# Kernel tuning notes

Hardware: AMD Instinct MI355X
Metric: run time of the kernel (lower is better)

The kernel has to match this reference:

```python
import jax, jax.numpy as jnp
import numpy as np

# dims: L layers, T steps, N envs, D d_model, H heads, DH d_head, M mem_len, DI d_inner
L, T, N, D, H, DH, M, DI = 6, 128, 32, 1024, 16, 64, 128, 4096


def _layer_norm(x, g, b, eps=1e-5):
    mu = jnp.mean(x, axis=-1, keepdims=True)
    var = jnp.mean(jnp.square(x - mu), axis=-1, keepdims=True)
    return (x - mu) * jax.lax.rsqrt(var + eps) * g + b


def _rel_shift(x):
    # x: (n, h, q, k) with k axis indexed by relative distance (k-1 .. 0)
    n, h, q, k = x.shape
    x = jnp.pad(x, ((0, 0), (0, 0), (0, 0), (1, 0)))
    x = x.reshape(n, h, k + 1, q)[:, :, 1:, :].reshape(n, h, q, k)
    return x


def setup_inputs() -> dict:
    key = jax.random.key(0)
    ks = jax.random.split(key, 16)
    s = 0.02
    inp = {
        "x": jax.random.normal(ks[0], (T * N, D), jnp.float32),
        "context": jax.random.normal(ks[1], (T * N, D), jnp.float32),
        "mems": jax.random.normal(ks[2], (L, N, M, D), jnp.float32),
        "masks": jnp.ones((T * N,), jnp.float32),
        "Wq": jax.random.normal(ks[3], (L, D, H * DH), jnp.float32) * s,
        "Wk": jax.random.normal(ks[4], (L, D, H * DH), jnp.float32) * s,
        "Wv": jax.random.normal(ks[5], (L, D, H * DH), jnp.float32) * s,
        "Wr": jax.random.normal(ks[6], (L, D, H * DH), jnp.float32) * s,
        "Wo": jax.random.normal(ks[7], (L, H * DH, D), jnp.float32) * s,
        "W1": jax.random.normal(ks[8], (L, D, DI), jnp.float32) * s,
        "b1": jnp.zeros((L, DI), jnp.float32),
        "W2": jax.random.normal(ks[9], (L, DI, D), jnp.float32) * s,
        "b2": jnp.zeros((L, D), jnp.float32),
        "ln1_g": jnp.ones((L, D), jnp.float32),
        "ln1_b": jnp.zeros((L, D), jnp.float32),
        "ln2_g": jnp.ones((L, D), jnp.float32),
        "ln2_b": jnp.zeros((L, D), jnp.float32),
        "r_w_bias": jax.random.normal(ks[10], (H, DH), jnp.float32) * s,
        "r_r_bias": jax.random.normal(ks[11], (H, DH), jnp.float32) * s,
    }
    return inp


def reference(x, context, mems, masks, Wq, Wk, Wv, Wr, Wo, W1, b1, W2, b2,
              ln1_g, ln1_b, ln2_g, ln2_b, r_w_bias, r_r_bias):
    n = mems.shape[1]
    t = x.shape[0] // n
    m = mems.shape[2]
    klen = m + t
    dh = r_w_bias.shape[-1]
    h_heads = r_w_bias.shape[0]

    xs = x.reshape(t, n, -1)
    ctx = context.reshape(t, n, -1)
    mk = masks.reshape(t, n)

    # zero memories for envs that reset at the first step (mems * masks)
    mems = mems * mk[0][None, :, None, None]

    # episode-reset attention mask: token i attends token j iff j<=i and no
    # reset (mask==0) happened between them; memory visible only before any reset
    ep = jnp.cumsum((mk == 0.0).astype(jnp.int32), axis=0)  # (t, n)
    epT = ep.T  # (n, t)
    causal = jnp.tril(jnp.ones((t, t), bool))
    allow_seq = causal[None, :, :] & (epT[:, :, None] == epT[:, None, :])  # (n,t,t)
    allow_mem = jnp.broadcast_to((epT == 0)[:, :, None], (n, t, m))  # (n,t,m)
    allow = jnp.concatenate([allow_mem, allow_seq], axis=-1)[:, None]  # (n,1,t,K)

    # sinusoidal relative position embedding, distances klen-1 .. 0
    pos = jnp.arange(klen - 1, -1, -1, dtype=x.dtype)
    inv_freq = 1.0 / (10000.0 ** (jnp.arange(0, xs.shape[-1], 2, dtype=x.dtype) / xs.shape[-1]))
    ang = pos[:, None] * inv_freq[None, :]
    R = jnp.concatenate([jnp.sin(ang), jnp.cos(ang)], axis=-1)  # (K, D)

    h = xs + ctx  # fuse observation features with goal context
    scale = 1.0 / jnp.sqrt(jnp.asarray(dh, x.dtype))

    n_layer = mems.shape[0]
    for l in range(n_layer):
        cat = jnp.concatenate([jnp.transpose(mems[l], (1, 0, 2)), h], axis=0)  # (K,n,D)
        q = (h @ Wq[l]).reshape(t, n, h_heads, dh)
        k = (cat @ Wk[l]).reshape(klen, n, h_heads, dh)
        v = (cat @ Wv[l]).reshape(klen, n, h_heads, dh)
        r = (R @ Wr[l]).reshape(klen, h_heads, dh)
        AC = jnp.einsum('inhd,jnhd->nhij', q + r_w_bias, k)
        BD = _rel_shift(jnp.einsum('inhd,jhd->nhij', q + r_r_bias, r))
        score = (AC + BD) * scale
        score = jnp.where(allow, score, -1e9)
        attn = jax.nn.softmax(score, axis=-1)
        o = jnp.einsum('nhij,jnhd->inhd', attn, v).reshape(t, n, h_heads * dh) @ Wo[l]
        h = _layer_norm(h + o, ln1_g[l], ln1_b[l])
        f = jax.nn.relu(h @ W1[l] + b1[l]) @ W2[l] + b2[l]
        h = _layer_norm(h + f, ln2_g[l], ln2_b[l])

    return h.reshape(t * n, -1)
```

## Files before the change

### kernel.cpp

```cpp
#include <hip/hip_runtime.h>
#include <stdint.h>

#define DEV static __device__ __forceinline__

typedef __attribute__((ext_vector_type(4))) float f32x4;
typedef __attribute__((ext_vector_type(8))) short bf16x8;
typedef __attribute__((ext_vector_type(4))) short s16x4;

static constexpr int L_ = 6, T_ = 128, NE = 32, D_ = 1024, H_ = 16, DH_ = 64, M_ = 128, DI_ = 4096;
static constexpr int KLEN = M_ + T_;
static constexpr int TN = T_ * NE;
static constexpr int NB = NE * H_;

DEV unsigned short f2bf(float f) {
  unsigned u = __builtin_bit_cast(unsigned, f);
  u += 0x7FFFu + ((u >> 16) & 1u);
  return (unsigned short)(u >> 16);
}
DEV float bf2f(unsigned short h) {
  unsigned u = ((unsigned)h) << 16;
  return __builtin_bit_cast(float, u);
}

DEV void gload16(const unsigned short* g, unsigned short* lds) {
  __builtin_amdgcn_global_load_lds(
      (const __attribute__((address_space(1))) unsigned int*)g,
      (__attribute__((address_space(3))) unsigned int*)lds, 16, 0, 0);
}

DEV void stage128(const unsigned short* __restrict__ Ab, int lda,
                  const unsigned short* __restrict__ Bb, int ldb,
                  unsigned short* lA, unsigned short* lB,
                  int m0, int n0, int k0, int w, int l)
{
#pragma unroll
  for (int i = 0; i < 4; ++i) {
    const int obb = i * 4096 + w * 1024;
    const int ob  = obb + (l << 4);
    const int row = ob >> 7;
    const int col = (((ob >> 4) & 7) ^ (row & 7)) << 3;
    gload16(Ab + (size_t)(m0 + row) * lda + k0 + col, lA + (obb >> 1));
    gload16(Bb + (size_t)(n0 + row) * ldb + k0 + col, lB + (obb >> 1));
  }
}

DEV void compute128(const unsigned short* lA, const unsigned short* lB,
                    int w, int l, f32x4 acc[4][4])
{
  const int wr = (w >> 1) * 64, wc = (w & 1) * 64;
  const int lan = l & 15, lgr = l >> 4;
#pragma unroll
  for (int ks = 0; ks < 2; ++ks) {
    bf16x8 av[4], bv[4];
#pragma unroll
    for (int m = 0; m < 4; ++m) {
      const int row = wr + m * 16 + lan;
      const int byte = ((row << 7) + (ks << 6) + (lgr << 4)) ^ ((row & 7) << 4);
      av[m] = *(const bf16x8*)((const char*)lA + byte);
    }
#pragma unroll
    for (int n = 0; n < 4; ++n) {
      const int row = wc + n * 16 + lan;
      const int byte = ((row << 7) + (ks << 6) + (lgr << 4)) ^ ((row & 7) << 4);
      bv[n] = *(const bf16x8*)((const char*)lB + byte);
    }
#pragma unroll
    for (int m = 0; m < 4; ++m)
#pragma unroll
      for (int n = 0; n < 4; ++n)
        acc[m][n] = __builtin_amdgcn_mfma_f32_16x16x32_bf16(av[m], bv[n], acc[m][n], 0, 0, 0);
  }
}

DEV void gemm128_2ph(const unsigned short* __restrict__ Ab, int lda,
                     const unsigned short* __restrict__ Bb, int ldb,
                     unsigned short (*shA)[8192], unsigned short (*shB)[8192],
                     int m0, int n0, int nK, int w, int l, f32x4 acc[4][4])
{
  stage128(Ab, lda, Bb, ldb, shA[0], shB[0], m0, n0, 0, w, l);
  asm volatile("s_waitcnt vmcnt(0)" ::: "memory");
  __syncthreads();
  int cur = 0;
  for (int kt = 0; kt < nK; ++kt) {
    if (kt + 1 < nK)
      stage128(Ab, lda, Bb, ldb, shA[cur ^ 1], shB[cur ^ 1], m0, n0, (kt + 1) * 64, w, l);
    compute128(shA[cur], shB[cur], w, l, acc);
    asm volatile("s_waitcnt vmcnt(0)" ::: "memory");
    __syncthreads();
    cur ^= 1;
  }
}

template <int EPI>
__global__ __launch_bounds__(256) void gemm_bt(
    const unsigned short* __restrict__ A, int lda, int sAn, int sAh,
    const unsigned short* __restrict__ B, int ldb, int sBn, int sBh,
    void* __restrict__ Cv, int ldc, int sC,
    const float* __restrict__ bias, int nK, int Hb)
{
  __shared__ unsigned short shA[2][8192];
  __shared__ unsigned short shB[2][8192];

  const int z = blockIdx.z;
  const int bn = z / Hb, bh = z % Hb;
  const unsigned short* Ab = A + (size_t)bn * sAn + (size_t)bh * sAh;
  const unsigned short* Bb = B + (size_t)bn * sBn + (size_t)bh * sBh;
  const int m0 = blockIdx.y * 128;
  const int n0 = blockIdx.x * 128;

  const int t = threadIdx.x;
  const int w = t >> 6, l = t & 63;
  const int wr = (w >> 1) * 64, wc = (w & 1) * 64;
  const int lan = l & 15, lgr = l >> 4;

  f32x4 acc[4][4];
#pragma unroll
  for (int m = 0; m < 4; ++m)
#pragma unroll
    for (int n = 0; n < 4; ++n) acc[m][n] = (f32x4){0.f, 0.f, 0.f, 0.f};

  gemm128_2ph(Ab, lda, Bb, ldb, shA, shB, m0, n0, nK, w, l, acc);

  const int zc = z * sC;
#pragma unroll
  for (int m = 0; m < 4; ++m) {
    const int row = m0 + wr + m * 16 + lgr * 4;
#pragma unroll
    for (int n = 0; n < 4; ++n) {
      const int col = n0 + wc + n * 16 + lan;
      const float bcol = (EPI >= 2) ? bias[col] : 0.f;
#pragma unroll
      for (int e = 0; e < 4; ++e) {
        float v = acc[m][n][e];
        const size_t idx = (size_t)zc + (size_t)(row + e) * ldc + col;
        if (EPI == 0) {
          ((float*)Cv)[idx] = v;
        } else if (EPI == 1) {
          ((unsigned short*)Cv)[idx] = f2bf(v);
        } else if (EPI == 2) {
          v += bcol; v = v > 0.f ? v : 0.f;
          ((unsigned short*)Cv)[idx] = f2bf(v);
        } else {
          ((float*)Cv)[idx] = v + bcol;
        }
      }
    }
  }
}

__global__ __launch_bounds__(256) void gemm_proj(
    const unsigned short* __restrict__ catA, const unsigned short* __restrict__ wt,
    unsigned short* __restrict__ kb, unsigned short* __restrict__ vb,
    unsigned short* __restrict__ qw, unsigned short* __restrict__ qr,
    unsigned short* __restrict__ rb,
    const float* __restrict__ rwb, const float* __restrict__ rrb)
{
  __shared__ unsigned short shA[2][8192];
  __shared__ unsigned short shB[2][8192];

  const int id = blockIdx.x;
  int by, bx;
  if (id < 1024)      { by = id >> 4;               bx = id & 15; }
  else if (id < 1280) { const int u = id - 1024; by = 32 + (u >> 3); bx = 16 + (u & 7); }
  else                { const int u = id - 1280; by = 64 + (u >> 3); bx = 24 + (u & 7); }
  const int m0 = by * 128, n0 = bx * 128;

  const int t = threadIdx.x;
  const int w = t >> 6, l = t & 63;
  const int wr = (w >> 1) * 64, wc = (w & 1) * 64;
  const int lan = l & 15, lgr = l >> 4;

  f32x4 acc[4][4];
#pragma unroll
  for (int m = 0; m < 4; ++m)
#pragma unroll
    for (int n = 0; n < 4; ++n) acc[m][n] = (f32x4){0.f, 0.f, 0.f, 0.f};

  gemm128_2ph(catA, 1024, wt, 1024, shA, shB, m0, n0, 16, w, l, acc);

#pragma unroll
  for (int m = 0; m < 4; ++m) {
    const int row = m0 + wr + m * 16 + lgr * 4;
#pragma unroll
    for (int n = 0; n < 4; ++n) {
      const int col = n0 + wc + n * 16 + lan;
#pragma unroll
      for (int e = 0; e < 4; ++e) {
        const float v = acc[m][n][e];
        const int r = row + e;
        if (col < 1024) {
          kb[(size_t)r * 1024 + col] = f2bf(v);
        } else if (col < 2048) {
          vb[(size_t)r * 1024 + col - 1024] = f2bf(v);
        } else if (col < 3072) {
          const int c = col - 2048;
          const size_t o = (size_t)(r - 4096) * 1024 + c;
          qw[o] = f2bf(v + rwb[c]);
          qr[o] = f2bf(v + rrb[c]);
        } else {
          const int c = col - 3072;
          rb[(size_t)(r - 8192) * 1024 + c] = f2bf(v);
        }
      }
    }
  }
}

__global__ __launch_bounds__(256) void gemm_scores(
    const unsigned short* __restrict__ qw, const unsigned short* __restrict__ qr,
    const unsigned short* __restrict__ kbf, const unsigned short* __restrict__ rbf,
    unsigned short* __restrict__ AC, unsigned short* __restrict__ BD)
{
  __shared__ unsigned short shA[2][8192];
  __shared__ unsigned short shB[2][8192];

  const int bx = blockIdx.x;
  const int z = blockIdx.y;
  const int nn = z >> 4, hh = z & 15;
  const bool isBD = bx >= 2;
  const int n0 = (bx & 1) * 128;
  const unsigned short* Ab = (isBD ? qr : qw) + (size_t)nn * 1024 + hh * 64;
  const unsigned short* Bb = isBD ? (rbf + hh * 64)
                                  : (kbf + (size_t)nn * 1024 + hh * 64);
  const int ldb = isBD ? 1024 : (NE * 1024);
  unsigned short* C = (isBD ? BD : AC) + (size_t)z * (T_ * KLEN);

  const int t = threadIdx.x;
  const int w = t >> 6, l = t & 63;
  const int wr = (w >> 1) * 64, wc = (w & 1) * 64;
  const int lan = l & 15, lgr = l >> 4;

  f32x4 acc[4][4];
#pragma unroll
  for (int m = 0; m < 4; ++m)
#pragma unroll
    for (int n = 0; n < 4; ++n) acc[m][n] = (f32x4){0.f, 0.f, 0.f, 0.f};

  gemm128_2ph(Ab, NE * 1024, Bb, ldb, shA, shB, 0, n0, 1, w, l, acc);

#pragma unroll
  for (int m = 0; m < 4; ++m) {
    const int row = wr + m * 16 + lgr * 4;
#pragma unroll
    for (int n = 0; n < 4; ++n) {
      const int col = n0 + wc + n * 16 + lan;
#pragma unroll
      for (int e = 0; e < 4; ++e)
        C[(size_t)(row + e) * KLEN + col] = f2bf(acc[m][n][e]);
    }
  }
}

__global__ __launch_bounds__(256) void smpv_kernel(
    const unsigned short* __restrict__ AC, const unsigned short* __restrict__ BD,
    const int* __restrict__ ep, const unsigned short* __restrict__ V,
    unsigned short* __restrict__ O)
{
  __shared__ unsigned short sP[128 * 256];

  const int z = blockIdx.x;
  const int nn = z >> 4, hh = z & 15;
  const int t = threadIdx.x, w = t >> 6, l = t & 63;
  const int lan = l & 15, lgr = l >> 4;
  const size_t zbase = (size_t)z * (T_ * KLEN);

  const int j0 = l * 4;
  for (int rr = 0; rr < 32; ++rr) {
    const int i = w * 32 + rr;
    const int epi = ep[i * NE + nn];
    const size_t base = zbase + (size_t)i * KLEN;
    s16x4 ac4 = *(const s16x4*)&AC[base + j0];
    float sc[4];
#pragma unroll
    for (int q = 0; q < 4; ++q) {
      const int j = j0 + q;
      int jx = j + (T_ - 1) - i; if (jx > KLEN - 1) jx = KLEN - 1;
      const float bd = bf2f((unsigned short)BD[base + jx]);
      bool allow;
      if (j < M_) {
        allow = (epi == 0);
      } else {
        const int jp = j - M_;
        allow = (jp <= i) && (ep[jp * NE + nn] == epi);
      }
      const float v = (bf2f((unsigned short)ac4[q]) + bd) * 0.125f;
      sc[q] = allow ? v : -1e9f;
    }
    float mx = fmaxf(fmaxf(sc[0], sc[1]), fmaxf(sc[2], sc[3]));
#pragma unroll
    for (int o = 32; o; o >>= 1) mx = fmaxf(mx, __shfl_xor(mx, o));
    float p[4], sum = 0.f;
#pragma unroll
    for (int q = 0; q < 4; ++q) { p[q] = __expf(sc[q] - mx); sum += p[q]; }
#pragma unroll
    for (int o = 32; o; o >>= 1) sum += __shfl_xor(sum, o);
    const float inv = 1.f / sum;
    s16x4 o4;
#pragma unroll
    for (int q = 0; q < 4; ++q) o4[q] = (short)f2bf(p[q] * inv);
    const int swz = ((i >> 2) & 3) * 16;
    *(s16x4*)&sP[i * 256 + (j0 ^ swz)] = o4;
  }
  __syncthreads();

  const int i0 = w * 32;
  const unsigned short* Vz = V + hh * DH_;

  f32x4 acc[2][4];
#pragma unroll
  for (int m = 0; m < 2; ++m)
#pragma unroll
    for (int n = 0; n < 4; ++n) acc[m][n] = (f32x4){0.f, 0.f, 0.f, 0.f};

  for (int ks = 0; ks < 8; ++ks) {
    const int kb = ks * 32 + lgr * 8;
    bf16x8 bv[4];
#pragma unroll
    for (int n = 0; n < 4; ++n) {
      const int d = n * 16 + lan;
      bf16x8 tmp;
#pragma unroll
      for (int jj = 0; jj < 8; ++jj)
        tmp[jj] = (short)Vz[(size_t)((kb + jj) * NE + nn) * 1024 + d];
      bv[n] = tmp;
    }
    bf16x8 av[2];
#pragma unroll
    for (int m = 0; m < 2; ++m) {
      const int row = i0 + m * 16 + lan;
      const int swz = ((row >> 2) & 3) * 16;
      av[m] = *(const bf16x8*)&sP[row * 256 + (kb ^ swz)];
    }
#pragma unroll
    for (int m = 0; m < 2; ++m)
#pragma unroll
      for (int n = 0; n < 4; ++n)
        acc[m][n] = __builtin_amdgcn_mfma_f32_16x16x32_bf16(av[m], bv[n], acc[m][n], 0, 0, 0);
  }
#pragma unroll
  for (int m = 0; m < 2; ++m)
#pragma unroll
    for (int n = 0; n < 4; ++n)
#pragma unroll
      for (int e = 0; e < 4; ++e) {
        const int i = i0 + m * 16 + lgr * 4 + e;
        const int d = n * 16 + lan;
        O[(size_t)(i * NE + nn) * 1024 + hh * DH_ + d] = f2bf(acc[m][n][e]);
      }
}

__global__ __launch_bounds__(256) void transpose_kernel(
    const float* __restrict__ W, unsigned short* __restrict__ WT, int Kd, int Nd)
{
  __shared__ float tile[32][33];
  const int tx = threadIdx.x & 31, ty = threadIdx.x >> 5;
  const int nIn = blockIdx.x * 32 + tx;
  const int kBase = blockIdx.y * 32;
#pragma unroll
  for (int r = 0; r < 32; r += 8)
    tile[ty + r][tx] = W[(size_t)(kBase + ty + r) * Nd + nIn];
  __syncthreads();
#pragma unroll
  for (int r = 0; r < 32; r += 8)
    WT[(size_t)(blockIdx.x * 32 + ty + r) * Kd + kBase + tx] = f2bf(tile[tx][ty + r]);
}

__global__ __launch_bounds__(256) void transpose5_kernel(
    const float* __restrict__ Wk, const float* __restrict__ Wv,
    const float* __restrict__ Wq, const float* __restrict__ Wr,
    const float* __restrict__ Wo,
// ... 31 lines not shown
    const float* __restrict__ x, const float* __restrict__ ctx,
    float* __restrict__ h, unsigned short* __restrict__ catUp)
{
  const int idx = blockIdx.x * 256 + threadIdx.x;
  const float v = x[idx] + ctx[idx];
  h[idx] = v;
  catUp[idx] = f2bf(v);
}

__global__ __launch_bounds__(256) void rpos_kernel(unsigned short* __restrict__ R)
{
  const int idx = blockIdx.x * 256 + threadIdx.x;
  const int d = idx & 1023, j = idx >> 10;
  const float pos = (float)(KLEN - 1 - j);
  const int f = d & 511;
  const float inv_freq = __expf(-((float)(2 * f) * (1.f / 1024.f)) * 9.210340371976184f);
  const float ang = pos * inv_freq;
  const float v = (d < 512) ? sinf(ang) : cosf(ang);
  R[idx] = f2bf(v);
}

__global__ void ep_kernel(const float* __restrict__ masks, int* __restrict__ ep)
{
  const int nn = threadIdx.x;
  if (nn < NE) {
    int c = 0;
    for (int i = 0; i < T_; ++i) {
      c += (masks[i * NE + nn] == 0.f) ? 1 : 0;
      ep[i * NE + nn] = c;
    }
  }
}

__global__ __launch_bounds__(256) void ln_kernel(
    const float* __restrict__ a, const float* __restrict__ p0,
    const float* __restrict__ p1, const float* __restrict__ bias,
    const float* __restrict__ g, const float* __restrict__ bb,
    float* __restrict__ outf, unsigned short* __restrict__ outbf)
{
  const int row = blockIdx.x;
  const int t = threadIdx.x, w = t >> 6, l = t & 63;
  const int c = t * 4;
  const size_t base = (size_t)row * 1024;
  f32x4 va = *(const f32x4*)&a[base + c];
  f32x4 v0 = *(const f32x4*)&p0[base + c];
  f32x4 v1 = *(const f32x4*)&p1[base + c];
  f32x4 v = va + v0 + v1;
  if (bias) {
    f32x4 vb = *(const f32x4*)&bias[c];
    v = v + vb;
  }
  float s = v[0] + v[1] + v[2] + v[3];
#pragma unroll
  for (int o = 32; o; o >>= 1) s += __shfl_xor(s, o);
  __shared__ float red[8];
  if (l == 0) red[w] = s;
  __syncthreads();
  s = red[0] + red[1] + red[2] + red[3];
  const float mu = s * (1.f / 1024.f);
  f32x4 dv = v - mu;
  float s2 = dv[0]*dv[0] + dv[1]*dv[1] + dv[2]*dv[2] + dv[3]*dv[3];
#pragma unroll
  for (int o = 32; o; o >>= 1) s2 += __shfl_xor(s2, o);
  if (l == 0) red[4 + w] = s2;
  __syncthreads();
  s2 = red[4] + red[5] + red[6] + red[7];
  const float inv = rsqrtf(s2 * (1.f / 1024.f) + 1e-5f);
  f32x4 y;
#pragma unroll
  for (int q = 0; q < 4; ++q) y[q] = dv[q] * inv * g[c + q] + bb[c + q];
  *(f32x4*)&outf[base + c] = y;
  if (outbf) {
    s16x4 o4;
#pragma unroll
    for (int q = 0; q < 4; ++q) o4[q] = (short)f2bf(y[q]);
    *(s16x4*)&outbf[base + c] = o4;
  }
}

extern "C" void kernel_launch(void* const* d_in, const int* in_sizes, int n_in,
                              void* d_out, int out_size, void* d_ws, size_t ws_size,
                              hipStream_t stream)
{
  (void)in_sizes; (void)n_in; (void)out_size; (void)ws_size;
// ... 8 lines not shown
  const float* Wo   = (const float*)d_in[8];
  const float* W1   = (const float*)d_in[9];
  const float* b1   = (const float*)d_in[10];
  const float* W2   = (const float*)d_in[11];
  const float* b2   = (const float*)d_in[12];
  const float* ln1g = (const float*)d_in[13];
  const float* ln1b = (const float*)d_in[14];
  const float* ln2g = (const float*)d_in[15];
  const float* ln2b = (const float*)d_in[16];
  const float* rwb  = (const float*)d_in[17];
  const float* rrb  = (const float*)d_in[18];

  char* ws = (char*)d_ws;
  size_t off = 0;
  auto alloc = [&](size_t bytes) {
    char* p = ws + off;
    off += (bytes + 255) & ~(size_t)255;
    return p;
  };
  unsigned short* wtAll = (unsigned short*)alloc(4096u * 1024 * 2);
  unsigned short* wto = (unsigned short*)alloc(1024u * 1024 * 2);
  unsigned short* wt1 = (unsigned short*)alloc(4096u * 1024 * 2);
  unsigned short* wt2 = (unsigned short*)alloc(4096u * 1024 * 2);
  unsigned short* cat = (unsigned short*)alloc((size_t)(KLEN * NE + 256) * 1024 * 2);
  unsigned short* rbf = (unsigned short*)alloc((size_t)KLEN * 1024 * 2);
  int*            epb = (int*)alloc((size_t)T_ * NE * 4);
  float*          h   = (float*)alloc((size_t)TN * 1024 * 4);
  float*          h1  = (float*)alloc((size_t)TN * 1024 * 4);
  unsigned short* qw  = (unsigned short*)alloc((size_t)TN * 1024 * 2);
  unsigned short* qr  = (unsigned short*)alloc((size_t)TN * 1024 * 2);
  unsigned short* kbf = (unsigned short*)alloc((size_t)KLEN * NE * 1024 * 2);
  unsigned short* vbf = (unsigned short*)alloc((size_t)KLEN * NE * 1024 * 2);
  unsigned short* ACb = (unsigned short*)alloc((size_t)NB * T_ * KLEN * 2);
  unsigned short* BDb = (unsigned short*)alloc((size_t)NB * T_ * KLEN * 2);
  unsigned short* obf = (unsigned short*)alloc((size_t)TN * 1024 * 2);

  unsigned short* catUp = cat + (size_t)M_ * NE * 1024;
  unsigned short* catR  = cat + (size_t)KLEN * NE * 1024;
  unsigned short* f1 = ACb;
  float* part = (float*)BDb;
  float* part1 = part + (size_t)TN * 1024;
  unsigned short* h1bf = qw;

  rpos_kernel<<<KLEN * 1024 / 256, 256, 0, stream>>>(catR);
  ep_kernel<<<1, 64, 0, stream>>>(masks, epb);
  hprep_kernel<<<TN * 1024 / 256, 256, 0, stream>>>(x, ctx, h, catUp);

  for (int l = 0; l < L_; ++l) {
    const size_t wOff = (size_t)l * 1024 * 1024;
    const size_t wOffBig = (size_t)l * 1024 * 4096;
    transpose5_kernel<<<dim3(32, 32, 5), 256, 0, stream>>>(
        Wk + wOff, Wv + wOff, Wq + wOff, Wr + wOff, Wo + wOff, wtAll, wto);
    transpose_kernel<<<dim3(128, 32), 256, 0, stream>>>(W1 + wOffBig, wt1, 1024, 4096);
    transpose_kernel<<<dim3(32, 128), 256, 0, stream>>>(W2 + wOffBig, wt2, 4096, 1024);
    catmem_kernel<<<M_ * NE * 1024 / 256, 256, 0, stream>>>(
        mems + (size_t)l * NE * M_ * 1024, masks, cat);

    gemm_proj<<<1296, 256, 0, stream>>>(cat, wtAll, kbf, vbf, qw, qr, rbf, rwb, rrb);

    gemm_scores<<<dim3(4, 512), 256, 0, stream>>>(qw, qr, kbf, rbf, ACb, BDb);

    smpv_kernel<<<NB, 256, 0, stream>>>(ACb, BDb, epb, vbf, obf);

    gemm_bt<0><<<dim3(8, 32, 2), 256, 0, stream>>>(obf, 1024, 0, 512,
                                                   wto, 1024, 0, 512,
                                                   part, 1024, TN * 1024, nullptr, 8, 2);
    ln_kernel<<<TN, 256, 0, stream>>>(h, part, part1, nullptr,
                                      ln1g + l * 1024, ln1b + l * 1024, h1, h1bf);

    gemm_bt<2><<<dim3(32, 32, 1), 256, 0, stream>>>(h1bf, 1024, 0, 0, wt1, 1024, 0, 0,
                                                    f1, 4096, 0, b1 + l * 4096, 16, 1);
    gemm_bt<0><<<dim3(8, 32, 2), 256, 0, stream>>>(f1, 4096, 0, 2048,
                                                   wt2, 4096, 0, 2048,
                                                   part, 1024, TN * 1024, nullptr, 32, 2);
    ln_kernel<<<TN, 256, 0, stream>>>(h1, part, part1, b2 + l * 1024,
                                      ln2g + l * 1024, ln2b + l * 1024,
                                      (l == L_ - 1) ? (float*)d_out : h, catUp);
  }
}
```

Baseline: 1.945 ms.

## Use pipelined 256x256 GEMM tiles for projection and FFN, split-K four ways

Adds a 512-thread GEMM that computes a 256x256 tile per block. It stages A and B in half-tiles, using a multi-phase loop that overlaps LDS fragment loads, async global-to-LDS copies and MFMA bursts under s_setprio. The fused QKV/R projection and both FFN GEMMs move to this kernel, raising data reuse per loaded byte. The W2 GEMM now splits K four ways, and a templated LayerNorm sums a variable number of partial buffers. The four partial buffers overrun the old scratch region and rely on a newly allocated buffer placed right after it; the larger tiles also mean fewer blocks and heavier register use per block.

```diff
diff --git a/kernel.cpp b/kernel.cpp
--- a/kernel.cpp
+++ b/kernel.cpp
@@ -28,162 +28,218 @@
       (__attribute__((address_space(3))) unsigned int*)lds, 16, 0, 0);
 }
 
-DEV void stage128(const unsigned short* __restrict__ Ab, int lda,
-                  const unsigned short* __restrict__ Bb, int ldb,
-                  unsigned short* lA, unsigned short* lB,
-                  int m0, int n0, int k0, int w, int l)
-{
-#pragma unroll
-  for (int i = 0; i < 4; ++i) {
-    const int obb = i * 4096 + w * 1024;
-    const int ob  = obb + (l << 4);
+#define WAITV4 asm volatile("s_waitcnt vmcnt(4)" ::: "memory")
+#define WAITV0 asm volatile("s_waitcnt vmcnt(0)" ::: "memory")
+#define BAR    asm volatile("s_barrier" ::: "memory")
+
+DEV void stage_half(const unsigned short* g, int ld, unsigned short* lbase, int t) {
+#pragma unroll
+  for (int r = 0; r < 2; ++r) {
+    const int obb = r * 8192 + (t >> 6) * 1024;
+    const int ob  = obb + ((t & 63) << 4);
     const int row = ob >> 7;
     const int col = (((ob >> 4) & 7) ^ (row & 7)) << 3;
-    gload16(Ab + (size_t)(m0 + row) * lda + k0 + col, lA + (obb >> 1));
-    gload16(Bb + (size_t)(n0 + row) * ldb + k0 + col, lB + (obb >> 1));
-  }
-}
-
-DEV void compute128(const unsigned short* lA, const unsigned short* lB,
-                    int w, int l, f32x4 acc[4][4])
-{
-  const int wr = (w >> 1) * 64, wc = (w & 1) * 64;
+    gload16(g + (size_t)row * ld + col, lbase + (obb >> 1));
+  }
+}
+
+DEV bf16x8 ldsfrag(const unsigned short* base, int row, int kk, int lgr) {
+  const int byte = ((row << 7) + (kk << 6) + (lgr << 4)) ^ ((row & 7) << 4);
+  return *(const bf16x8*)((const char*)base + byte);
+}
+
+DEV void gemm256_pipe(const unsigned short* __restrict__ Ab, int lda,
+                      const unsigned short* __restrict__ Bb, int ldb,
+                      unsigned short* lds, int m0, int n0, int NT, int t,
+                      f32x4 acc[8][4])
+{
+  const int w = t >> 6, l = t & 63;
+  const int wm = w >> 2, wn = w & 3;
   const int lan = l & 15, lgr = l >> 4;
-#pragma unroll
-  for (int ks = 0; ks < 2; ++ks) {
-    bf16x8 av[4], bv[4];
-#pragma unroll
-    for (int m = 0; m < 4; ++m) {
-      const int row = wr + m * 16 + lan;
-      const int byte = ((row << 7) + (ks << 6) + (lgr << 4)) ^ ((row & 7) << 4);
-      av[m] = *(const bf16x8*)((const char*)lA + byte);
-    }
+
+  unsigned short* A0h[2] = { lds + 0,              lds + 32768 };
+  unsigned short* A1h[2] = { lds + 8192,           lds + 32768 + 8192 };
+  unsigned short* B0h[2] = { lds + 16384,          lds + 32768 + 16384 };
+  unsigned short* B1h[2] = { lds + 16384 + 8192,   lds + 32768 + 16384 + 8192 };
+
+  stage_half(Bb + (size_t)n0 * ldb,              ldb, B0h[0], t);
+  stage_half(Bb + (size_t)(n0 + 128) * ldb,      ldb, B1h[0], t);
+  stage_half(Ab + (size_t)m0 * lda,              lda, A0h[0], t);
+  stage_half(Ab + (size_t)(m0 + 128) * lda,      lda, A1h[0], t);
+  if (NT > 1) {
+    stage_half(Bb + (size_t)n0 * ldb + 64,       ldb, B0h[1], t);
+    stage_half(Bb + (size_t)(n0 + 128) * ldb + 64, ldb, B1h[1], t);
+    WAITV4;
+  } else {
+    WAITV0;
+  }
+  BAR;
+
+  for (int kt = 0; kt < NT; ++kt) {
+    const int p = kt & 1;
+    const unsigned short* A_ = (wm == 0) ? A0h[p] : A1h[p];
+    const unsigned short* B_ = ((wn >> 1) == 0) ? B0h[p] : B1h[p];
+    const int br0 = (wn & 1) * 64;
+    bf16x8 av[8], bv[8];
+
+#pragma unroll
+    for (int m = 0; m < 4; ++m)
+#pragma unroll
+      for (int kk = 0; kk < 2; ++kk)
+        av[m * 2 + kk] = ldsfrag(A_, m * 16 + lan, kk, lgr);
+#pragma unroll
+    for (int n = 0; n < 2; ++n)
+#pragma unroll
+      for (int kk = 0; kk < 2; ++kk)
+        bv[n * 2 + kk] = ldsfrag(B_, br0 + n * 16 + lan, kk, lgr);
+    if (kt + 1 < NT)
+      stage_half(Ab + (size_t)m0 * lda + (kt + 1) * 64, lda, A0h[p ^ 1], t);
+    BAR;
+    __builtin_amdgcn_s_setprio(1);
+#pragma unroll
+    for (int m = 0; m < 4; ++m)
+#pragma unroll
+      for (int n = 0; n < 2; ++n)
+#pragma unroll
+        for (int kk = 0; kk < 2; ++kk)
+          acc[m][n] = __builtin_amdgcn_mfma_f32_16x16x32_bf16(av[m*2+kk], bv[n*2+kk], acc[m][n], 0, 0, 0);
+    __builtin_amdgcn_s_setprio(0);
+    BAR;
+
+#pragma unroll
+    for (int n = 0; n < 2; ++n)
+#pragma unroll
+      for (int kk = 0; kk < 2; ++kk)
+        bv[4 + n * 2 + kk] = ldsfrag(B_, br0 + 32 + n * 16 + lan, kk, lgr);
+    if (kt + 1 < NT)
+      stage_half(Ab + (size_t)(m0 + 128) * lda + (kt + 1) * 64, lda, A1h[p ^ 1], t);
+    BAR;
+    __builtin_amdgcn_s_setprio(1);
+#pragma unroll
+    for (int m = 0; m < 4; ++m)
+#pragma unroll
+      for (int n = 0; n < 2; ++n)
+#pragma unroll
+        for (int kk = 0; kk < 2; ++kk)
+          acc[m][2 + n] = __builtin_amdgcn_mfma_f32_16x16x32_bf16(av[m*2+kk], bv[4+n*2+kk], acc[m][2+n], 0, 0, 0);
+    __builtin_amdgcn_s_setprio(0);
+    BAR;
+
+#pragma unroll
+    for (int m = 0; m < 4; ++m)
+#pragma unroll
+      for (int kk = 0; kk < 2; ++kk)
+        av[m * 2 + kk] = ldsfrag(A_, 64 + m * 16 + lan, kk, lgr);
+    if (kt + 2 < NT)
+      stage_half(Bb + (size_t)n0 * ldb + (kt + 2) * 64, ldb, B0h[p], t);
+    BAR;
+    __builtin_amdgcn_s_setprio(1);
+#pragma unroll
+    for (int m = 0; m < 4; ++m)
+#pragma unroll
+      for (int n = 0; n < 2; ++n)
+#pragma unroll
+        for (int kk = 0; kk < 2; ++kk)
+          acc[4 + m][2 + n] = __builtin_amdgcn_mfma_f32_16x16x32_bf16(av[m*2+kk], bv[4+n*2+kk], acc[4+m][2+n], 0, 0, 0);
+    __builtin_amdgcn_s_setprio(0);
+    BAR;
+
+    if (kt + 2 < NT)
+      stage_half(Bb + (size_t)(n0 + 128) * ldb + (kt + 2) * 64, ldb, B1h[p], t);
+    if (kt + 2 < NT) { WAITV4; }
+    else if (kt + 1 < NT) { WAITV0; }
+    BAR;
+    __builtin_amdgcn_s_setprio(1);
+#pragma unroll
+    for (int m = 0; m < 4; ++m)
+#pragma unroll
+      for (int n = 0; n < 2; ++n)
+#pragma unroll
+        for (int kk = 0; kk < 2; ++kk)
+          acc[4 + m][n] = __builtin_amdgcn_mfma_f32_16x16x32_bf16(av[m*2+kk], bv[n*2+kk], acc[4+m][n], 0, 0, 0);
+    __builtin_amdgcn_s_setprio(0);
+    BAR;
+  }
+}
+
+template <int EPI>
+__global__ __launch_bounds__(512) void gemm256_bt(
+    const unsigned short* __restrict__ A, int lda, int sAh,
+    const unsigned short* __restrict__ B, int ldb, int sBh,
+    void* __restrict__ Cv, int ldc, int sC,
+    const float* __restrict__ bias, int nK)
+{
+  __shared__ unsigned short lds[65536];
+  const int z = blockIdx.z;
+  const int m0 = blockIdx.y * 256, n0 = blockIdx.x * 256;
+  const int t = threadIdx.x;
+
+  f32x4 acc[8][4];
+#pragma unroll
+  for (int m = 0; m < 8; ++m)
+#pragma unroll
+    for (int n = 0; n < 4; ++n) acc[m][n] = (f32x4){0.f, 0.f, 0.f, 0.f};
+
+  gemm256_pipe(A + (size_t)z * sAh, lda, B + (size_t)z * sBh, ldb,
+               lds, m0, n0, nK, t, acc);
+
+  const int w = t >> 6, l = t & 63;
+  const int wm = w >> 2, wn = w & 3, lan = l & 15, lgr = l >> 4;
+  const size_t zc = (size_t)z * sC;
+#pragma unroll
+  for (int m = 0; m < 8; ++m) {
+    const int row = m0 + wm * 128 + m * 16 + lgr * 4;
 #pragma unroll
     for (int n = 0; n < 4; ++n) {
-      const int row = wc + n * 16 + lan;
-      const int byte = ((row << 7) + (ks << 6) + (lgr << 4)) ^ ((row & 7) << 4);
-      bv[n] = *(const bf16x8*)((const char*)lB + byte);
-    }
-#pragma unroll
-    for (int m = 0; m < 4; ++m)
-#pragma unroll
-      for (int n = 0; n < 4; ++n)
-        acc[m][n] = __builtin_amdgcn_mfma_f32_16x16x32_bf16(av[m], bv[n], acc[m][n], 0, 0, 0);
-  }
-}
-
-DEV void gemm128_2ph(const unsigned short* __restrict__ Ab, int lda,
-                     const unsigned short* __restrict__ Bb, int ldb,
-                     unsigned short (*shA)[8192], unsigned short (*shB)[8192],
-                     int m0, int n0, int nK, int w, int l, f32x4 acc[4][4])
-{
-  stage128(Ab, lda, Bb, ldb, shA[0], shB[0], m0, n0, 0, w, l);
-  asm volatile("s_waitcnt vmcnt(0)" ::: "memory");
-  __syncthreads();
-  int cur = 0;
-  for (int kt = 0; kt < nK; ++kt) {
-    if (kt + 1 < nK)
-      stage128(Ab, lda, Bb, ldb, shA[cur ^ 1], shB[cur ^ 1], m0, n0, (kt + 1) * 64, w, l);
-    compute128(shA[cur], shB[cur], w, l, acc);
-    asm volatile("s_waitcnt vmcnt(0)" ::: "memory");
-    __syncthreads();
-    cur ^= 1;
-  }
-}
-
-template <int EPI>
-__global__ __launch_bounds__(256) void gemm_bt(
-    const unsigned short* __restrict__ A, int lda, int sAn, int sAh,
-    const unsigned short* __restrict__ B, int ldb, int sBn, int sBh,
-    void* __restrict__ Cv, int ldc, int sC,
-    const float* __restrict__ bias, int nK, int Hb)
-{
-  __shared__ unsigned short shA[2][8192];
-  __shared__ unsigned short shB[2][8192];
-
-  const int z = blockIdx.z;
-  const int bn = z / Hb, bh = z % Hb;
-  const unsigned short* Ab = A + (size_t)bn * sAn + (size_t)bh * sAh;
-  const unsigned short* Bb = B + (size_t)bn * sBn + (size_t)bh * sBh;
-  const int m0 = blockIdx.y * 128;
-  const int n0 = blockIdx.x * 128;
-
-  const int t = threadIdx.x;
-  const int w = t >> 6, l = t & 63;
-  const int wr = (w >> 1) * 64, wc = (w & 1) * 64;
-  const int lan = l & 15, lgr = l >> 4;
-
-  f32x4 acc[4][4];
-#pragma unroll
-  for (int m = 0; m < 4; ++m)
-#pragma unroll
-    for (int n = 0; n < 4; ++n) acc[m][n] = (f32x4){0.f, 0.f, 0.f, 0.f};
-
-  gemm128_2ph(Ab, lda, Bb, ldb, shA, shB, m0, n0, nK, w, l, acc);
-
-  const int zc = z * sC;
-#pragma unroll
-  for (int m = 0; m < 4; ++m) {
-    const int row = m0 + wr + m * 16 + lgr * 4;
-#pragma unroll
-    for (int n = 0; n < 4; ++n) {
-      const int col = n0 + wc + n * 16 + lan;
+      const int col = n0 + wn * 64 + n * 16 + lan;
       const float bcol = (EPI >= 2) ? bias[col] : 0.f;
 #pragma unroll
       for (int e = 0; e < 4; ++e) {
         float v = acc[m][n][e];
-        const size_t idx = (size_t)zc + (size_t)(row + e) * ldc + col;
+        const size_t idx = zc + (size_t)(row + e) * ldc + col;
         if (EPI == 0) {
           ((float*)Cv)[idx] = v;
-        } else if (EPI == 1) {
-          ((unsigned short*)Cv)[idx] = f2bf(v);
-        } else if (EPI == 2) {
+        } else {
           v += bcol; v = v > 0.f ? v : 0.f;
           ((unsigned short*)Cv)[idx] = f2bf(v);
-        } else {
-          ((float*)Cv)[idx] = v + bcol;
         }
       }
     }
   }
 }
 
-__global__ __launch_bounds__(256) void gemm_proj(
+__global__ __launch_bounds__(512) void gemm256_proj(
     const unsigned short* __restrict__ catA, const unsigned short* __restrict__ wt,
     unsigned short* __restrict__ kb, unsigned short* __restrict__ vb,
     unsigned short* __restrict__ qw, unsigned short* __restrict__ qr,
     unsigned short* __restrict__ rb,
     const float* __restrict__ rwb, const float* __restrict__ rrb)
 {
-  __shared__ unsigned short shA[2][8192];
-  __shared__ unsigned short shB[2][8192];
-
+  __shared__ unsigned short lds[65536];
   const int id = blockIdx.x;
   int by, bx;
-  if (id < 1024)      { by = id >> 4;               bx = id & 15; }
-  else if (id < 1280) { const int u = id - 1024; by = 32 + (u >> 3); bx = 16 + (u & 7); }
-  else                { const int u = id - 1280; by = 64 + (u >> 3); bx = 24 + (u & 7); }
-  const int m0 = by * 128, n0 = bx * 128;
-
+  if (id < 256)      { by = id >> 3;                 bx = id & 7; }
+  else if (id < 320) { const int u = id - 256; by = 16 + (u >> 2); bx = 8 + (u & 3); }
+  else               { const int u = id - 320; by = 32;            bx = 12 + (u & 3); }
+  const int m0 = by * 256, n0 = bx * 256;
   const int t = threadIdx.x;
+
+  f32x4 acc[8][4];
+#pragma unroll
+  for (int m = 0; m < 8; ++m)
+#pragma unroll
+    for (int n = 0; n < 4; ++n) acc[m][n] = (f32x4){0.f, 0.f, 0.f, 0.f};
+
+  gemm256_pipe(catA, 1024, wt, 1024, lds, m0, n0, 16, t, acc);
+
   const int w = t >> 6, l = t & 63;
-  const int wr = (w >> 1) * 64, wc = (w & 1) * 64;
-  const int lan = l & 15, lgr = l >> 4;
-
-  f32x4 acc[4][4];
-#pragma unroll
-  for (int m = 0; m < 4; ++m)
-#pragma unroll
-    for (int n = 0; n < 4; ++n) acc[m][n] = (f32x4){0.f, 0.f, 0.f, 0.f};
-
-  gemm128_2ph(catA, 1024, wt, 1024, shA, shB, m0, n0, 16, w, l, acc);
-
-#pragma unroll
-  for (int m = 0; m < 4; ++m) {
-    const int row = m0 + wr + m * 16 + lgr * 4;
+  const int wm = w >> 2, wn = w & 3, lan = l & 15, lgr = l >> 4;
+#pragma unroll
+  for (int m = 0; m < 8; ++m) {
+    const int row = m0 + wm * 128 + m * 16 + lgr * 4;
 #pragma unroll
     for (int n = 0; n < 4; ++n) {
-      const int col = n0 + wc + n * 16 + lan;
+      const int col = n0 + wn * 64 + n * 16 + lan;
 #pragma unroll
       for (int e = 0; e < 4; ++e) {
         const float v = acc[m][n][e];
@@ -206,13 +262,133 @@
   }
 }
 
+DEV void stage128(const unsigned short* __restrict__ Ab, int lda,
+                  const unsigned short* __restrict__ Bb, int ldb,
+                  unsigned short* lA, unsigned short* lB,
+                  int m0, int n0, int k0, int w, int l)
+{
+#pragma unroll
+  for (int i = 0; i < 4; ++i) {
+    const int obb = i * 4096 + w * 1024;
+    const int ob  = obb + (l << 4);
+    const int row = ob >> 7;
+    const int col = (((ob >> 4) & 7) ^ (row & 7)) << 3;
+    gload16(Ab + (size_t)(m0 + row) * lda + k0 + col, lA + (obb >> 1));
+    gload16(Bb + (size_t)(n0 + row) * ldb + k0 + col, lB + (obb >> 1));
+  }
+}
+
+DEV void compute128(const unsigned short* lA, const unsigned short* lB,
+                    int w, int l, f32x4 acc[4][4])
+{
+  const int wr = (w >> 1) * 64, wc = (w & 1) * 64;
+  const int lan = l & 15, lgr = l >> 4;
+#pragma unroll
+  for (int ks = 0; ks < 2; ++ks) {
+    bf16x8 av[4], bv[4];
+#pragma unroll
+    for (int m = 0; m < 4; ++m) {
+      const int row = wr + m * 16 + lan;
+      const int byte = ((row << 7) + (ks << 6) + (lgr << 4)) ^ ((row & 7) << 4);
+      av[m] = *(const bf16x8*)((const char*)lA + byte);
+    }
+#pragma unroll
+    for (int n = 0; n < 4; ++n) {
+      const int row = wc + n * 16 + lan;
+      const int byte = ((row << 7) + (ks << 6) + (lgr << 4)) ^ ((row & 7) << 4);
+      bv[n] = *(const bf16x8*)((const char*)lB + byte);
+    }
+#pragma unroll
+    for (int m = 0; m < 4; ++m)
+#pragma unroll
+      for (int n = 0; n < 4; ++n)
+        acc[m][n] = __builtin_amdgcn_mfma_f32_16x16x32_bf16(av[m], bv[n], acc[m][n], 0, 0, 0);
+  }
+}
+
+DEV void gemm128_2ph(const unsigned short* __restrict__ Ab, int lda,
+                     const unsigned short* __restrict__ Bb, int ldb,
+                     unsigned short (*shA)[8192], unsigned short (*shB)[8192],
+                     int m0, int n0, int nK, int w, int l, f32x4 acc[4][4])
+{
+  stage128(Ab, lda, Bb, ldb, shA[0], shB[0], m0, n0, 0, w, l);
+  WAITV0;
+  __syncthreads();
+  int cur = 0;
+  for (int kt = 0; kt < nK; ++kt) {
+    if (kt + 1 < nK)
+      stage128(Ab, lda, Bb, ldb, shA[cur ^ 1], shB[cur ^ 1], m0, n0, (kt + 1) * 64, w, l);
+    compute128(shA[cur], shB[cur], w, l, acc);
+    WAITV0;
+    __syncthreads();
+    cur ^= 1;
+  }
+}
+
+template <int EPI>
+__global__ __launch_bounds__(256) void gemm_bt(
+    const unsigned short* __restrict__ A, int lda, int sAn, int sAh,
+    const unsigned short* __restrict__ B, int ldb, int sBn, int sBh,
+    void* __restrict__ Cv, int ldc, int sC,
+    const float* __restrict__ bias, int nK, int Hb)
+{
+  __shared__ unsigned short shA[2][8192];
+  __shared__ unsigned short shB[2][8192];
+
+  const int z = blockIdx.z;
+  const int bn = z / Hb, bh = z % Hb;
+  const unsigned short* Ab = A + (size_t)bn * sAn + (size_t)bh * sAh;
+  const unsigned short* Bb = B + (size_t)bn * sBn + (size_t)bh * sBh;
+  const int m0 = blockIdx.y * 128;
+  const int n0 = blockIdx.x * 128;
+
+  const int t = threadIdx.x;
+  const int w = t >> 6, l = t & 63;
+  const int wr = (w >> 1) * 64, wc = (w & 1) * 64;
+  const int lan = l & 15, lgr = l >> 4;
+
+  f32x4 acc[4][4];
+#pragma unroll
+  for (int m = 0; m < 4; ++m)
+#pragma unroll
+    for (int n = 0; n < 4; ++n) acc[m][n] = (f32x4){0.f, 0.f, 0.f, 0.f};
+
+  gemm128_2ph(Ab, lda, Bb, ldb, shA, shB, m0, n0, nK, w, l, acc);
+
+  const int zc = z * sC;
+#pragma unroll
+  for (int m = 0; m < 4; ++m) {
+    const int row = m0 + wr + m * 16 + lgr * 4;
+#pragma unroll
+    for (int n = 0; n < 4; ++n) {
+      const int col = n0 + wc + n * 16 + lan;
+      const float bcol = (EPI >= 2) ? bias[col] : 0.f;
+#pragma unroll
+      for (int e = 0; e < 4; ++e) {
+        float v = acc[m][n][e];
+        const size_t idx = (size_t)zc + (size_t)(row + e) * ldc + col;
+        if (EPI == 0) {
+          ((float*)Cv)[idx] = v;
+        } else if (EPI == 1) {
+          ((unsigned short*)Cv)[idx] = f2bf(v);
+        } else if (EPI == 2) {
+          v += bcol; v = v > 0.f ? v : 0.f;
+          ((unsigned short*)Cv)[idx] = f2bf(v);
+        } else {
+          ((float*)Cv)[idx] = v + bcol;
+        }
+      }
+    }
+  }
+}
+
 __global__ __launch_bounds__(256) void gemm_scores(
     const unsigned short* __restrict__ qw, const unsigned short* __restrict__ qr,
     const unsigned short* __restrict__ kbf, const unsigned short* __restrict__ rbf,
     unsigned short* __restrict__ AC, unsigned short* __restrict__ BD)
 {
-  __shared__ unsigned short shA[2][8192];
-  __shared__ unsigned short shB[2][8192];
+  __shared__ unsigned short shA[8192];
+  __shared__ unsigned short shB[8192];
 
   const int bx = blockIdx.x;
   const int z = blockIdx.y;
@@ -236,7 +412,10 @@
 #pragma unroll
     for (int n = 0; n < 4; ++n) acc[m][n] = (f32x4){0.f, 0.f, 0.f, 0.f};
 
-  gemm128_2ph(Ab, NE * 1024, Bb, ldb, shA, shB, 0, n0, 1, w, l, acc);
+  stage128(Ab, NE * 1024, Bb, ldb, shA, shB, 0, n0, 0, w, l);
+  WAITV0;
+  __syncthreads();
+  compute128(shA, shB, w, l, acc);
 
 #pragma unroll
   for (int m = 0; m < 4; ++m) {
@@ -433,9 +612,10 @@
   }
 }
 
+template <int NP>
 __global__ __launch_bounds__(256) void ln_kernel(
-    const float* __restrict__ a, const float* __restrict__ p0,
-    const float* __restrict__ p1, const float* __restrict__ bias,
+    const float* __restrict__ a, const float* __restrict__ parts, size_t pstride,
+    const float* __restrict__ bias,
     const float* __restrict__ g, const float* __restrict__ bb,
     float* __restrict__ outf, unsigned short* __restrict__ outbf)
 {
@@ -443,14 +623,11 @@
   const int t = threadIdx.x, w = t >> 6, l = t & 63;
   const int c = t * 4;
   const size_t base = (size_t)row * 1024;
-  f32x4 va = *(const f32x4*)&a[base + c];
-  f32x4 v0 = *(const f32x4*)&p0[base + c];
-  f32x4 v1 = *(const f32x4*)&p1[base + c];
-  f32x4 v = va + v0 + v1;
-  if (bias) {
-    f32x4 vb = *(const f32x4*)&bias[c];
-    v = v + vb;
-  }
+  f32x4 v = *(const f32x4*)&a[base + c];
+#pragma unroll
+  for (int i = 0; i < NP; ++i)
+    v = v + *(const f32x4*)&parts[i * pstride + base + c];
+  if (bias) v = v + *(const f32x4*)&bias[c];
   float s = v[0] + v[1] + v[2] + v[3];
 #pragma unroll
   for (int o = 32; o; o >>= 1) s += __shfl_xor(s, o);
@@ -525,14 +702,15 @@
   unsigned short* kbf = (unsigned short*)alloc((size_t)KLEN * NE * 1024 * 2);
   unsigned short* vbf = (unsigned short*)alloc((size_t)KLEN * NE * 1024 * 2);
   unsigned short* ACb = (unsigned short*)alloc((size_t)NB * T_ * KLEN * 2);
+  unsigned short* obf = (unsigned short*)alloc((size_t)TN * 1024 * 2);
   unsigned short* BDb = (unsigned short*)alloc((size_t)NB * T_ * KLEN * 2);
-  unsigned short* obf = (unsigned short*)alloc((size_t)TN * 1024 * 2);
-
+  float*          pex = (float*)alloc((size_t)2 * TN * 1024 * 4);
+
+  (void)pex;
   unsigned short* catUp = cat + (size_t)M_ * NE * 1024;
   unsigned short* catR  = cat + (size_t)KLEN * NE * 1024;
   unsigned short* f1 = ACb;
   float* part = (float*)BDb;
-  float* part1 = part + (size_t)TN * 1024;
   unsigned short* h1bf = qw;
 
   rpos_kernel<<<KLEN * 1024 / 256, 256, 0, stream>>>(catR);
@@ -549,7 +727,7 @@
     catmem_kernel<<<M_ * NE * 1024 / 256, 256, 0, stream>>>(
         mems + (size_t)l * NE * M_ * 1024, masks, cat);
 
-    gemm_proj<<<1296, 256, 0, stream>>>(cat, wtAll, kbf, vbf, qw, qr, rbf, rwb, rrb);
+    gemm256_proj<<<324, 512, 0, stream>>>(cat, wtAll, kbf, vbf, qw, qr, rbf, rwb, rrb);
 
     gemm_scores<<<dim3(4, 512), 256, 0, stream>>>(qw, qr, kbf, rbf, ACb, BDb);
 
@@ -558,16 +736,17 @@
     gemm_bt<0><<<dim3(8, 32, 2), 256, 0, stream>>>(obf, 1024, 0, 512,
                                                    wto, 1024, 0, 512,
                                                    part, 1024, TN * 1024, nullptr, 8, 2);
-    ln_kernel<<<TN, 256, 0, stream>>>(h, part, part1, nullptr,
-                                      ln1g + l * 1024, ln1b + l * 1024, h1, h1bf);
-
-    gemm_bt<2><<<dim3(32, 32, 1), 256, 0, stream>>>(h1bf, 1024, 0, 0, wt1, 1024, 0, 0,
-                                                    f1, 4096, 0, b1 + l * 4096, 16, 1);
-    gemm_bt<0><<<dim3(8, 32, 2), 256, 0, stream>>>(f1, 4096, 0, 2048,
-                                                   wt2, 4096, 0, 2048,
-                                                   part, 1024, TN * 1024, nullptr, 32, 2);
-    ln_kernel<<<TN, 256, 0, stream>>>(h1, part, part1, b2 + l * 1024,
-                                      ln2g + l * 1024, ln2b + l * 1024,
-                                      (l == L_ - 1) ? (float*)d_out : h, catUp);
-  }
-}
+    ln_kernel<2><<<TN, 256, 0, stream>>>(h, part, (size_t)TN * 1024, nullptr,
+                                         ln1g + l * 1024, ln1b + l * 1024, h1, h1bf);
+
+    gemm256_bt<2><<<dim3(16, 16, 1), 512, 0, stream>>>(
+        h1bf, 1024, 0, wt1, 1024, 0,
+        f1, 4096, 0, b1 + l * 4096, 16);
+    gemm256_bt<0><<<dim3(4, 16, 4), 512, 0, stream>>>(
+        f1, 4096, 1024, wt2, 4096, 1024,
+        part, 1024, TN * 1024, nullptr, 16);
+    ln_kernel<4><<<TN, 256, 0, stream>>>(h1, part, (size_t)TN * 1024, b2 + l * 1024,
+                                         ln2g + l * 1024, ln2b + l * 1024,
+                                         (l == L_ - 1) ? (float*)d_out : h, catUp);
+  }
+}
```

Measured after the change: 3.348 ms. 72.1% more time.

## Fuse score GEMMs into attention kernel, keeping AC+BD scores in LDS

Applied to the files above, without the earlier changes.

Merges the separate AC/BD score GEMM kernel into the softmax-PV kernel. Each wave computes its 32 query rows of AC and the relative-shifted BD directly with MFMA from global q/k/r and accumulates them into a per-wave LDS score tile. This removes the global write and read of the two large bf16 score buffers and one launch per layer. In exchange, K and R are loaded from global without LDS staging and are reread by every wave. The BD add rounds through bf16 in LDS. The layernorm kernel is also generalized to take a templated count of partial buffers.

```diff
diff --git a/kernel.cpp b/kernel.cpp
--- a/kernel.cpp
+++ b/kernel.cpp
@@ -27,6 +27,8 @@
       (const __attribute__((address_space(1))) unsigned int*)g,
       (__attribute__((address_space(3))) unsigned int*)lds, 16, 0, 0);
 }
+
+#define WAITV0 asm volatile("s_waitcnt vmcnt(0)" ::: "memory")
 
 DEV void stage128(const unsigned short* __restrict__ Ab, int lda,
                   const unsigned short* __restrict__ Bb, int ldb,
@@ -78,14 +80,14 @@
                      int m0, int n0, int nK, int w, int l, f32x4 acc[4][4])
 {
   stage128(Ab, lda, Bb, ldb, shA[0], shB[0], m0, n0, 0, w, l);
-  asm volatile("s_waitcnt vmcnt(0)" ::: "memory");
+  WAITV0;
   __syncthreads();
   int cur = 0;
   for (int kt = 0; kt < nK; ++kt) {
     if (kt + 1 < nK)
       stage128(Ab, lda, Bb, ldb, shA[cur ^ 1], shB[cur ^ 1], m0, n0, (kt + 1) * 64, w, l);
     compute128(shA[cur], shB[cur], w, l, acc);
-    asm volatile("s_waitcnt vmcnt(0)" ::: "memory");
+    WAITV0;
     __syncthreads();
     cur ^= 1;
   }
@@ -206,76 +208,100 @@
   }
 }
 
-__global__ __launch_bounds__(256) void gemm_scores(
+__global__ __launch_bounds__(256) void attn_kernel(
     const unsigned short* __restrict__ qw, const unsigned short* __restrict__ qr,
     const unsigned short* __restrict__ kbf, const unsigned short* __restrict__ rbf,
-    unsigned short* __restrict__ AC, unsigned short* __restrict__ BD)
-{
-  __shared__ unsigned short shA[2][8192];
-  __shared__ unsigned short shB[2][8192];
-
-  const int bx = blockIdx.x;
-  const int z = blockIdx.y;
-  const int nn = z >> 4, hh = z & 15;
-  const bool isBD = bx >= 2;
-  const int n0 = (bx & 1) * 128;
-  const unsigned short* Ab = (isBD ? qr : qw) + (size_t)nn * 1024 + hh * 64;
-  const unsigned short* Bb = isBD ? (rbf + hh * 64)
-                                  : (kbf + (size_t)nn * 1024 + hh * 64);
-  const int ldb = isBD ? 1024 : (NE * 1024);
-  unsigned short* C = (isBD ? BD : AC) + (size_t)z * (T_ * KLEN);
-
-  const int t = threadIdx.x;
-  const int w = t >> 6, l = t & 63;
-  const int wr = (w >> 1) * 64, wc = (w & 1) * 64;
-  const int lan = l & 15, lgr = l >> 4;
-
-  f32x4 acc[4][4];
-#pragma unroll
-  for (int m = 0; m < 4; ++m)
-#pragma unroll
-    for (int n = 0; n < 4; ++n) acc[m][n] = (f32x4){0.f, 0.f, 0.f, 0.f};
-
-  gemm128_2ph(Ab, NE * 1024, Bb, ldb, shA, shB, 0, n0, 1, w, l, acc);
-
-#pragma unroll
-  for (int m = 0; m < 4; ++m) {
-    const int row = wr + m * 16 + lgr * 4;
-#pragma unroll
-    for (int n = 0; n < 4; ++n) {
-      const int col = n0 + wc + n * 16 + lan;
-#pragma unroll
-      for (int e = 0; e < 4; ++e)
-        C[(size_t)(row + e) * KLEN + col] = f2bf(acc[m][n][e]);
-    }
-  }
-}
-
-__global__ __launch_bounds__(256) void smpv_kernel(
-    const unsigned short* __restrict__ AC, const unsigned short* __restrict__ BD,
     const int* __restrict__ ep, const unsigned short* __restrict__ V,
     unsigned short* __restrict__ O)
 {
-  __shared__ unsigned short sP[128 * 256];
+  __shared__ unsigned short sS[4][32 * 256];
 
   const int z = blockIdx.x;
   const int nn = z >> 4, hh = z & 15;
   const int t = threadIdx.x, w = t >> 6, l = t & 63;
   const int lan = l & 15, lgr = l >> 4;
-  const size_t zbase = (size_t)z * (T_ * KLEN);
+  const int i0 = w * 32;
+  unsigned short* S = sS[w];
+
+  bf16x8 av[2][2];
+#pragma unroll
+  for (int m = 0; m < 2; ++m)
+#pragma unroll
+    for (int kk = 0; kk < 2; ++kk) {
+      const int i = i0 + m * 16 + lan;
+      av[m][kk] = *(const bf16x8*)&qw[(size_t)(i * NE + nn) * 1024 + hh * 64 + kk * 32 + lgr * 8];
+    }
+#pragma unroll
+  for (int n = 0; n < 16; ++n) {
+    bf16x8 bv[2];
+#pragma unroll
+    for (int kk = 0; kk < 2; ++kk) {
+      const int j = n * 16 + lan;
+      bv[kk] = *(const bf16x8*)&kbf[(size_t)(j * NE + nn) * 1024 + hh * 64 + kk * 32 + lgr * 8];
+    }
+#pragma unroll
+    for (int m = 0; m < 2; ++m) {
+      f32x4 a4 = (f32x4){0.f, 0.f, 0.f, 0.f};
+#pragma unroll
+      for (int kk = 0; kk < 2; ++kk)
+        a4 = __builtin_amdgcn_mfma_f32_16x16x32_bf16(av[m][kk], bv[kk], a4, 0, 0, 0);
+#pragma unroll
+      for (int e = 0; e < 4; ++e) {
+        const int r = m * 16 + lgr * 4 + e;
+        const int j = n * 16 + lan;
+        const int swz = ((r >> 2) & 3) * 16;
+        S[r * 256 + (j ^ swz)] = f2bf(a4[e]);
+      }
+    }
+  }
+
+  bf16x8 bq[2][2];
+#pragma unroll
+  for (int m = 0; m < 2; ++m)
+#pragma unroll
+    for (int kk = 0; kk < 2; ++kk) {
+      const int i = i0 + m * 16 + lan;
+      bq[m][kk] = *(const bf16x8*)&qr[(size_t)(i * NE + nn) * 1024 + hh * 64 + kk * 32 + lgr * 8];
+    }
+#pragma unroll
+  for (int n = 0; n < 16; ++n) {
+    bf16x8 bv[2];
+#pragma unroll
+    for (int kk = 0; kk < 2; ++kk) {
+      const int jp = n * 16 + lan;
+      bv[kk] = *(const bf16x8*)&rbf[(size_t)jp * 1024 + hh * 64 + kk * 32 + lgr * 8];
+    }
+#pragma unroll
+    for (int m = 0; m < 2; ++m) {
+      f32x4 a4 = (f32x4){0.f, 0.f, 0.f, 0.f};
+#pragma unroll
+      for (int kk = 0; kk < 2; ++kk)
+        a4 = __builtin_amdgcn_mfma_f32_16x16x32_bf16(bq[m][kk], bv[kk], a4, 0, 0, 0);
+#pragma unroll
+      for (int e = 0; e < 4; ++e) {
+        const int r = m * 16 + lgr * 4 + e;
+        const int i = i0 + r;
+        const int jp = n * 16 + lan;
+        const int j = jp + i - 127;
+        if (j >= 0 && j < 256) {
+          const int swz = ((r >> 2) & 3) * 16;
+          const int idx = r * 256 + (j ^ swz);
+          S[idx] = f2bf(bf2f(S[idx]) + a4[e]);
+        }
+      }
+    }
+  }
 
   const int j0 = l * 4;
   for (int rr = 0; rr < 32; ++rr) {
-    const int i = w * 32 + rr;
+    const int i = i0 + rr;
     const int epi = ep[i * NE + nn];
-    const size_t base = zbase + (size_t)i * KLEN;
-    s16x4 ac4 = *(const s16x4*)&AC[base + j0];
+    const int swz = ((rr >> 2) & 3) * 16;
+    s16x4 s4 = *(const s16x4*)&S[rr * 256 + (j0 ^ swz)];
     float sc[4];
 #pragma unroll
     for (int q = 0; q < 4; ++q) {
       const int j = j0 + q;
-      int jx = j + (T_ - 1) - i; if (jx > KLEN - 1) jx = KLEN - 1;
-      const float bd = bf2f((unsigned short)BD[base + jx]);
       bool allow;
       if (j < M_) {
         allow = (epi == 0);
@@ -283,8 +309,7 @@
         const int jp = j - M_;
         allow = (jp <= i) && (ep[jp * NE + nn] == epi);
       }
-      const float v = (bf2f((unsigned short)ac4[q]) + bd) * 0.125f;
-      sc[q] = allow ? v : -1e9f;
+      sc[q] = allow ? bf2f((unsigned short)s4[q]) * 0.125f : -1e9f;
     }
     float mx = fmaxf(fmaxf(sc[0], sc[1]), fmaxf(sc[2], sc[3]));
 #pragma unroll
@@ -298,14 +323,10 @@
     s16x4 o4;
 #pragma unroll
     for (int q = 0; q < 4; ++q) o4[q] = (short)f2bf(p[q] * inv);
-    const int swz = ((i >> 2) & 3) * 16;
-    *(s16x4*)&sP[i * 256 + (j0 ^ swz)] = o4;
-  }
-  __syncthreads();
-
-  const int i0 = w * 32;
+    *(s16x4*)&S[rr * 256 + (j0 ^ swz)] = o4;
+  }
+
   const unsigned short* Vz = V + hh * DH_;
-
   f32x4 acc[2][4];
 #pragma unroll
   for (int m = 0; m < 2; ++m)
@@ -314,7 +335,7 @@
 
   for (int ks = 0; ks < 8; ++ks) {
     const int kb = ks * 32 + lgr * 8;
-    bf16x8 bv[4];
+    bf16x8 bv2[4];
 #pragma unroll
     for (int n = 0; n < 4; ++n) {
       const int d = n * 16 + lan;
@@ -322,20 +343,20 @@
 #pragma unroll
       for (int jj = 0; jj < 8; ++jj)
         tmp[jj] = (short)Vz[(size_t)((kb + jj) * NE + nn) * 1024 + d];
-      bv[n] = tmp;
-    }
-    bf16x8 av[2];
+      bv2[n] = tmp;
+    }
+    bf16x8 pa[2];
 #pragma unroll
     for (int m = 0; m < 2; ++m) {
-      const int row = i0 + m * 16 + lan;
-      const int swz = ((row >> 2) & 3) * 16;
-      av[m] = *(const bf16x8*)&sP[row * 256 + (kb ^ swz)];
+      const int r = m * 16 + lan;
+      const int swz = ((r >> 2) & 3) * 16;
+      pa[m] = *(const bf16x8*)&S[r * 256 + (kb ^ swz)];
     }
 #pragma unroll
     for (int m = 0; m < 2; ++m)
 #pragma unroll
       for (int n = 0; n < 4; ++n)
-        acc[m][n] = __builtin_amdgcn_mfma_f32_16x16x32_bf16(av[m], bv[n], acc[m][n], 0, 0, 0);
+        acc[m][n] = __builtin_amdgcn_mfma_f32_16x16x32_bf16(pa[m], bv2[n], acc[m][n], 0, 0, 0);
   }
 #pragma unroll
   for (int m = 0; m < 2; ++m)
@@ -433,9 +454,10 @@
   }
 }
 
+template <int NP>
 __global__ __launch_bounds__(256) void ln_kernel(
-    const float* __restrict__ a, const float* __restrict__ p0,
-    const float* __restrict__ p1, const float* __restrict__ bias,
+    const float* __restrict__ a, const float* __restrict__ parts, size_t pstride,
+    const float* __restrict__ bias,
     const float* __restrict__ g, const float* __restrict__ bb,
     float* __restrict__ outf, unsigned short* __restrict__ outbf)
 {
@@ -443,14 +465,11 @@
   const int t = threadIdx.x, w = t >> 6, l = t & 63;
   const int c = t * 4;
   const size_t base = (size_t)row * 1024;
-  f32x4 va = *(const f32x4*)&a[base + c];
-  f32x4 v0 = *(const f32x4*)&p0[base + c];
-  f32x4 v1 = *(const f32x4*)&p1[base + c];
-  f32x4 v = va + v0 + v1;
-  if (bias) {
-    f32x4 vb = *(const f32x4*)&bias[c];
-    v = v + vb;
-  }
+  f32x4 v = *(const f32x4*)&a[base + c];
+#pragma unroll
+  for (int i = 0; i < NP; ++i)
+    v = v + *(const f32x4*)&parts[i * pstride + base + c];
+  if (bias) v = v + *(const f32x4*)&bias[c];
   float s = v[0] + v[1] + v[2] + v[3];
 #pragma unroll
   for (int o = 32; o; o >>= 1) s += __shfl_xor(s, o);
@@ -532,7 +551,6 @@
   unsigned short* catR  = cat + (size_t)KLEN * NE * 1024;
   unsigned short* f1 = ACb;
   float* part = (float*)BDb;
-  float* part1 = part + (size_t)TN * 1024;
   unsigned short* h1bf = qw;
 
   rpos_kernel<<<KLEN * 1024 / 256, 256, 0, stream>>>(catR);
@@ -551,23 +569,21 @@
 
     gemm_proj<<<1296, 256, 0, stream>>>(cat, wtAll, kbf, vbf, qw, qr, rbf, rwb, rrb);
 
-    gemm_scores<<<dim3(4, 512), 256, 0, stream>>>(qw, qr, kbf, rbf, ACb, BDb);
-
-    smpv_kernel<<<NB, 256, 0, stream>>>(ACb, BDb, epb, vbf, obf);
+    attn_kernel<<<NB, 256, 0, stream>>>(qw, qr, kbf, rbf, epb, vbf, obf);
 
     gemm_bt<0><<<dim3(8, 32, 2), 256, 0, stream>>>(obf, 1024, 0, 512,
                                                    wto, 1024, 0, 512,
                                                    part, 1024, TN * 1024, nullptr, 8, 2);
-    ln_kernel<<<TN, 256, 0, stream>>>(h, part, part1, nullptr,
-                                      ln1g + l * 1024, ln1b + l * 1024, h1, h1bf);
+    ln_kernel<2><<<TN, 256, 0, stream>>>(h, part, (size_t)TN * 1024, nullptr,
+                                         ln1g + l * 1024, ln1b + l * 1024, h1, h1bf);
 
     gemm_bt<2><<<dim3(32, 32, 1), 256, 0, stream>>>(h1bf, 1024, 0, 0, wt1, 1024, 0, 0,
                                                     f1, 4096, 0, b1 + l * 4096, 16, 1);
     gemm_bt<0><<<dim3(8, 32, 2), 256, 0, stream>>>(f1, 4096, 0, 2048,
                                                    wt2, 4096, 0, 2048,
                                                    part, 1024, TN * 1024, nullptr, 32, 2);
-    ln_kernel<<<TN, 256, 0, stream>>>(h1, part, part1, b2 + l * 1024,
-                                      ln2g + l * 1024, ln2b + l * 1024,
-                                      (l == L_ - 1) ? (float*)d_out : h, catUp);
-  }
-}
+    ln_kernel<2><<<TN, 256, 0, stream>>>(h1, part, (size_t)TN * 1024, b2 + l * 1024,
+                                         ln2g + l * 1024, ln2b + l * 1024,
+                                         (l == L_ - 1) ? (float*)d_out : h, catUp);
+  }
+}
```

After: 1.912 ms. No clear change (-1.7%).
